# Kernel optimization log

Hardware: AMD Instinct MI355X
Metric: run time of the kernel (lower is better)

Reference implementation:

```python
import jax, jax.numpy as jnp
import numpy as np

H = 8        # heads
W = 64       # window size
SHIFT = True
DIM = 512
SCALE = (DIM // H) ** -0.5


def setup_inputs() -> dict:
    key = jax.random.key(0)
    k1, k2, k3, k4 = jax.random.split(key, 4)
    x = jax.random.normal(k1, (8, 4096, DIM), dtype=jnp.float32)
    w_qkv = jax.random.normal(k2, (3 * DIM, DIM), dtype=jnp.float32) * 0.02
    w_proj = jax.random.normal(k3, (DIM, DIM), dtype=jnp.float32) * 0.02
    b_proj = jax.random.normal(k4, (DIM,), dtype=jnp.float32) * 0.02
    return {"x": x, "w_qkv": w_qkv, "w_proj": w_proj, "b_proj": b_proj}


def reference(x, w_qkv, w_proj, b_proj):
    B, N, C = x.shape
    if SHIFT:
        x = jnp.roll(x, -W // 2, axis=1)
    pad = (W - N % W) % W  # static Python int
    if pad:
        x = jnp.pad(x, ((0, 0), (0, pad), (0, 0)))
    nw = x.shape[1] // W
    xw = x.reshape(B * nw, W, C)                     # (B', W, C)
    qkv = xw @ w_qkv.T                               # (B', W, 3C)
    qkv = qkv.reshape(B * nw, W, 3, H, C // H)
    q, k, v = qkv[:, :, 0], qkv[:, :, 1], qkv[:, :, 2]  # (B', W, H, dh)
    # NOTE: faithful to source -- heads are NOT moved before matmul, so
    # attention is over the head axis: attn shape (B', W, H, H).
    attn = jnp.einsum('bwhd,bwgd->bwhg', q, k) * SCALE
    attn = jax.nn.softmax(attn, axis=-1)
    out = jnp.einsum('bwhg,bwgd->bwhd', attn, v)     # (B', W, H, dh)
    # transpose(1,2) then raw reshape, exactly as torch does (channel scramble)
    out = out.transpose(0, 2, 1, 3).reshape(B * nw, W, C)
    out = out @ w_proj.T + b_proj
    out = out.reshape(B, nw * W, C)[:, :N]
    if SHIFT:
        out = jnp.roll(out, W // 2, axis=1)
    return out
```

## Files before the change

kernel.cpp:

```cpp
#include <hip/hip_runtime.h>
#include <math.h>

typedef __attribute__((ext_vector_type(8))) short short8;
typedef __attribute__((ext_vector_type(4))) float float4v;

#define KDIM  512
#define NQKV  1536

__device__ __forceinline__ unsigned short f2bf(float f) {
    unsigned int u = __float_as_uint(f);
    u += 0x7FFFu + ((u >> 16) & 1u);
    return (unsigned short)(u >> 16);
}
__device__ __forceinline__ float bf2f(unsigned short u) {
    return __uint_as_float(((unsigned int)u) << 16);
}

__device__ __forceinline__ void gl2lds16(const unsigned short* g, unsigned short* l) {
    __builtin_amdgcn_global_load_lds(
        (const __attribute__((address_space(1))) void*)g,
        (__attribute__((address_space(3))) void*)l, 16, 0, 0);
}

__global__ __launch_bounds__(256) void cast_all_kernel(const float* __restrict__ x,
                                                       const float* __restrict__ wqkv,
                                                       const float* __restrict__ wproj,
                                                       unsigned short* __restrict__ xb,
                                                       unsigned short* __restrict__ wqkvb,
                                                       unsigned short* __restrict__ wprojb) {
    if (blockIdx.x < 16384) {
        int tid = blockIdx.x * 256 + threadIdx.x;
        int t = tid >> 7;
        int c = (tid & 127) << 2;
        int b = t >> 12, n = t & 4095;
        int src = (b << 12) | ((n + 32) & 4095);
        float4 v = *(const float4*)(x + (((size_t)src) << 9) + c);
        ushort4 o;
        o.x = f2bf(v.x); o.y = f2bf(v.y); o.z = f2bf(v.z); o.w = f2bf(v.w);
        *(ushort4*)(xb + (((size_t)t) << 9) + c) = o;
    } else {
        int tid = (blockIdx.x - 16384) * 256 + threadIdx.x;
        int e = tid << 2;
        if (e < NQKV * KDIM) {
            float4 v = *(const float4*)(wqkv + e);
            ushort4 o; o.x = f2bf(v.x); o.y = f2bf(v.y); o.z = f2bf(v.z); o.w = f2bf(v.w);
            *(ushort4*)(wqkvb + e) = o;
        } else {
            int e2 = e - NQKV * KDIM;
            float4 v = *(const float4*)(wproj + e2);
            ushort4 o; o.x = f2bf(v.x); o.y = f2bf(v.y); o.z = f2bf(v.z); o.w = f2bf(v.w);
            *(ushort4*)(wprojb + e2) = o;
        }
    }
}

template<int N>
__global__ __launch_bounds__(256, 2) void gemm_kernel(
        const unsigned short* __restrict__ A,
        const unsigned short* __restrict__ B,
        unsigned short* __restrict__ Cb) {
    __shared__ __align__(16) unsigned short As[128 * 64];
    __shared__ __align__(16) unsigned short Bs[128 * 64];
    constexpr int GX  = N / 128;
    constexpr int PER = (GX * 256) / 8;
    const int wgid = blockIdx.y * GX + blockIdx.x;
    const int swz  = (wgid & 7) * PER + (wgid >> 3);
    const int bm = swz / GX;
    const int bn = swz % GX;

    const int tid = threadIdx.x;
    const int wave = tid >> 6, lane = tid & 63;
    const int quad = lane >> 4, l16 = lane & 15;
    const int wm = (wave >> 1) * 64, wn = (wave & 1) * 64;
    const int srow = lane >> 3;
    const int scol = ((lane & 7) ^ srow) * 8;

    float4v acc[4][4] = {};

    const unsigned short* Abase = A + (size_t)(bm * 128) * KDIM;
    const unsigned short* Bbase = B + (size_t)(bn * 128) * KDIM;

    for (int k0 = 0; k0 < KDIM; k0 += 64) {
        #pragma unroll
        for (int j = 0; j < 4; j++) {
            int chunk = j * 4 + wave;
            int row = chunk * 8 + srow;
            gl2lds16(Abase + (size_t)row * KDIM + k0 + scol, As + chunk * 512);
            gl2lds16(Bbase + (size_t)row * KDIM + k0 + scol, Bs + chunk * 512);
        }
        __syncthreads();
        #pragma unroll
        for (int ki = 0; ki < 2; ki++) {
            short8 af[4], bf[4];
            #pragma unroll
            for (int mi = 0; mi < 4; mi++) {
                int r = wm + mi * 16 + l16;
                int blk = (ki * 4 + quad) ^ (l16 & 7);
                af[mi] = *(const short8*)(As + r * 64 + blk * 8);
            }
            #pragma unroll
            for (int ni = 0; ni < 4; ni++) {
                int r = wn + ni * 16 + l16;
                int blk = (ki * 4 + quad) ^ (l16 & 7);
                bf[ni] = *(const short8*)(Bs + r * 64 + blk * 8);
            }
            #pragma unroll
            for (int mi = 0; mi < 4; mi++)
                #pragma unroll
                for (int ni = 0; ni < 4; ni++)
                    acc[mi][ni] = __builtin_amdgcn_mfma_f32_16x16x32_bf16(
                        af[mi], bf[ni], acc[mi][ni], 0, 0, 0);
        }
        __syncthreads();
    }

    #pragma unroll
    for (int mi = 0; mi < 4; mi++) {
        #pragma unroll
        for (int r = 0; r < 4; r++) {
            int m = bm * 128 + wm + mi * 16 + quad * 4 + r;
            #pragma unroll
            for (int ni = 0; ni < 4; ni++) {
                int n = bn * 128 + wn + ni * 16 + l16;
                Cb[(size_t)m * N + n] = f2bf(acc[mi][ni][r]);
            }
        }
    }
}

#define KVS 1032
__global__ __launch_bounds__(512, 4) void attnproj_kernel(
        const unsigned short* __restrict__ qkvb,
        const unsigned short* __restrict__ wprojb,
        const float* __restrict__ bias,
        float* __restrict__ out) {
    __shared__ __align__(16) unsigned short Asf[32 * 512];
    __shared__ __align__(16) unsigned short KV[16 * KVS];
    const int tid = threadIdx.x;
    const int bid = blockIdx.x;
    const int swzb = (bid & 7) * 128 + (bid >> 3);
    const int win = swzb >> 1, half = swzb & 1;

    {
        const int dq = tid & 7;
        const int h  = (tid >> 3) & 3;
        const int tl = tid >> 5;
        const int hg = half * 4 + h;

        short8 qs[4];
        #pragma unroll
        for (int c = 0; c < 4; c++)
            qs[c] = *(const short8*)(qkvb + (size_t)(win * 64 + c * 16 + tl) * NQKV
                                     + hg * 64 + dq * 8);

        #pragma unroll
        for (int c = 0; c < 4; c++) {
            #pragma unroll
            for (int i = 0; i < 4; i++) {
                int slot = i * 512 + tid;
                int row = slot >> 7, c8 = slot & 127;
                gl2lds16(qkvb + (size_t)(win * 64 + c * 16 + row) * NQKV + 512 + c8 * 8,
                         KV + row * KVS + c8 * 8);
            }
            __syncthreads();

            const unsigned short* krow = KV + tl * KVS;
            const int w = c * 16 + tl;

            float qv[8];
            #pragma unroll
            for (int j = 0; j < 8; j++)
                qv[j] = bf2f((unsigned short)qs[c][j]);

            float s[8];
            #pragma unroll
            for (int g = 0; g < 8; g++) {
                float acc = 0.f;
                short8 ks = *(const short8*)(krow + g * 64 + dq * 8);
                #pragma unroll
                for (int j = 0; j < 8; j++)
                    acc += qv[j] * bf2f((unsigned short)ks[j]);
                acc += __shfl_xor(acc, 1);
                acc += __shfl_xor(acc, 2);
                acc += __shfl_xor(acc, 4);
                s[g] = acc;
            }

            float mx = s[0];
            #pragma unroll
            for (int g = 1; g < 8; g++) mx = fmaxf(mx, s[g]);
            float p[8], sum = 0.f;
            #pragma unroll
            for (int g = 0; g < 8; g++) { p[g] = __expf((s[g] - mx) * 0.125f); sum += p[g]; }
            float inv = 1.f / sum;
            #pragma unroll
            for (int g = 0; g < 8; g++) p[g] *= inv;

            float o[8];
            #pragma unroll
            for (int j = 0; j < 8; j++) o[j] = 0.f;
            #pragma unroll
            for (int g = 0; g < 8; g++) {
                short8 vs = *(const short8*)(krow + 512 + g * 64 + dq * 8);
                #pragma unroll
                for (int j = 0; j < 8; j++)
                    o[j] += p[g] * bf2f((unsigned short)vs[j]);
            }

            int r = h * 8 + (w >> 3);
            int keyr = (r ^ (r >> 3)) & 7;
            short8 pk;
            #pragma unroll
            for (int j = 0; j < 8; j++) pk[j] = (short)f2bf(o[j]);
            int cb = (w & 7) * 8 + dq;
            *(short8*)(Asf + r * 512 + ((cb ^ keyr) * 8)) = pk;
            __syncthreads();
        }
    }

    const int wave = tid >> 6, lane = tid & 63;
    const int quad = lane >> 4, l16 = lane & 15;
    const int wc = wave;

    float4v acc[2][4] = {};
    #pragma unroll
    for (int ks = 0; ks < 16; ks++) {
        short8 af[2], bfr[4];
        #pragma unroll
        for (int mi = 0; mi < 2; mi++) {
            int r = mi * 16 + l16;
            int kb = ks * 4 + quad;
            af[mi] = *(const short8*)(Asf + r * 512 + ((kb ^ ((r ^ (r >> 3)) & 7)) * 8));
        }
        #pragma unroll
        for (int ni = 0; ni < 4; ni++) {
            int r = wc * 64 + ni * 16 + l16;
            bfr[ni] = *(const short8*)(wprojb + (size_t)r * KDIM + ks * 32 + quad * 8);
        }
        #pragma unroll
        for (int mi = 0; mi < 2; mi++)
            #pragma unroll
            for (int ni = 0; ni < 4; ni++)
                acc[mi][ni] = __builtin_amdgcn_mfma_f32_16x16x32_bf16(
                    af[mi], bfr[ni], acc[mi][ni], 0, 0, 0);
    }

    #pragma unroll
    for (int mi = 0; mi < 2; mi++) {
        #pragma unroll
        for (int r4 = 0; r4 < 4; r4++) {
            int m = win * 64 + half * 32 + mi * 16 + quad * 4 + r4;
            int b = m >> 12, pp = m & 4095;
            int nrow = (pp + 32) & 4095;
            float* orow = out + (((size_t)((b << 12) | nrow)) << 9);
            #pragma unroll
            for (int ni = 0; ni < 4; ni++) {
                int n = wc * 64 + ni * 16 + l16;
                orow[n] = acc[mi][ni][r4] + bias[n];
            }
        }
    }
}

extern "C" void kernel_launch(void* const* d_in, const int* in_sizes, int n_in,
                              void* d_out, int out_size, void* d_ws, size_t ws_size,
                              hipStream_t stream) {
    const float* x      = (const float*)d_in[0];
    const float* w_qkv  = (const float*)d_in[1];
    const float* w_proj = (const float*)d_in[2];
    const float* b_proj = (const float*)d_in[3];
    float* out = (float*)d_out;

    char* ws = (char*)d_ws;
    unsigned short* xb     = (unsigned short*)(ws);
    unsigned short* wqkvb  = (unsigned short*)(ws + 33554432);
    unsigned short* wprojb = (unsigned short*)(ws + 35127296);
    unsigned short* qkvb   = (unsigned short*)(ws + 35651584);

    cast_all_kernel<<<17408, 256, 0, stream>>>(x, w_qkv, w_proj, xb, wqkvb, wprojb);
    gemm_kernel<NQKV><<<dim3(12, 256), 256, 0, stream>>>(xb, wqkvb, qkvb);
    attnproj_kernel<<<1024, 512, 0, stream>>>(qkvb, wprojb, b_proj, out);
}
```

Baseline: 256.5 us.

## Process whole window per block, interleaving attention and projection per chunk

Each block now handles one whole 64-token window with all 8 heads instead of half a window, so K/V rows are loaded once rather than twice. Attention output for each 16-token chunk is projected right away through a 16-row MFMA GEMM, and the next chunk's K/V load to LDS is issued before that GEMM so the two overlap. K/V LDS rows are XOR-swizzled instead of padded, and bias is hoisted into registers. The cost is half as many blocks, more register use, and reloading w_proj from global once per chunk.

```diff
diff --git a/kernel.cpp b/kernel.cpp
--- a/kernel.cpp
+++ b/kernel.cpp
@@ -128,137 +128,149 @@
     }
 }
 
-#define KVS 1032
 __global__ __launch_bounds__(512, 4) void attnproj_kernel(
         const unsigned short* __restrict__ qkvb,
         const unsigned short* __restrict__ wprojb,
         const float* __restrict__ bias,
         float* __restrict__ out) {
-    __shared__ __align__(16) unsigned short Asf[32 * 512];
-    __shared__ __align__(16) unsigned short KV[16 * KVS];
+    __shared__ __align__(16) unsigned short Asf[16 * 512];
+    __shared__ __align__(16) unsigned short KV[16 * 1024];
     const int tid = threadIdx.x;
     const int bid = blockIdx.x;
-    const int swzb = (bid & 7) * 128 + (bid >> 3);
-    const int win = swzb >> 1, half = swzb & 1;
-
-    {
-        const int dq = tid & 7;
-        const int h  = (tid >> 3) & 3;
-        const int tl = tid >> 5;
-        const int hg = half * 4 + h;
-
-        short8 qs[4];
-        #pragma unroll
-        for (int c = 0; c < 4; c++)
-            qs[c] = *(const short8*)(qkvb + (size_t)(win * 64 + c * 16 + tl) * NQKV
-                                     + hg * 64 + dq * 8);
-
-        #pragma unroll
-        for (int c = 0; c < 4; c++) {
-            #pragma unroll
-            for (int i = 0; i < 4; i++) {
-                int slot = i * 512 + tid;
-                int row = slot >> 7, c8 = slot & 127;
-                gl2lds16(qkvb + (size_t)(win * 64 + c * 16 + row) * NQKV + 512 + c8 * 8,
-                         KV + row * KVS + c8 * 8);
-            }
-            __syncthreads();
-
-            const unsigned short* krow = KV + tl * KVS;
-            const int w = c * 16 + tl;
-
-            float qv[8];
-            #pragma unroll
-            for (int j = 0; j < 8; j++)
-                qv[j] = bf2f((unsigned short)qs[c][j]);
-
-            float s[8];
-            #pragma unroll
-            for (int g = 0; g < 8; g++) {
-                float acc = 0.f;
-                short8 ks = *(const short8*)(krow + g * 64 + dq * 8);
-                #pragma unroll
-                for (int j = 0; j < 8; j++)
-                    acc += qv[j] * bf2f((unsigned short)ks[j]);
-                acc += __shfl_xor(acc, 1);
-                acc += __shfl_xor(acc, 2);
-                acc += __shfl_xor(acc, 4);
-                s[g] = acc;
-            }
-
-            float mx = s[0];
-            #pragma unroll
-            for (int g = 1; g < 8; g++) mx = fmaxf(mx, s[g]);
-            float p[8], sum = 0.f;
-            #pragma unroll
-            for (int g = 0; g < 8; g++) { p[g] = __expf((s[g] - mx) * 0.125f); sum += p[g]; }
-            float inv = 1.f / sum;
-            #pragma unroll
-            for (int g = 0; g < 8; g++) p[g] *= inv;
-
-            float o[8];
-            #pragma unroll
-            for (int j = 0; j < 8; j++) o[j] = 0.f;
-            #pragma unroll
-            for (int g = 0; g < 8; g++) {
-                short8 vs = *(const short8*)(krow + 512 + g * 64 + dq * 8);
-                #pragma unroll
-                for (int j = 0; j < 8; j++)
-                    o[j] += p[g] * bf2f((unsigned short)vs[j]);
-            }
-
-            int r = h * 8 + (w >> 3);
-            int keyr = (r ^ (r >> 3)) & 7;
-            short8 pk;
-            #pragma unroll
-            for (int j = 0; j < 8; j++) pk[j] = (short)f2bf(o[j]);
-            int cb = (w & 7) * 8 + dq;
-            *(short8*)(Asf + r * 512 + ((cb ^ keyr) * 8)) = pk;
-            __syncthreads();
-        }
-    }
+    const int win = (bid & 7) * 64 + (bid >> 3);
+
+    const int dq = tid & 3;
+    const int h  = (tid >> 2) & 7;
+    const int tl = tid >> 5;
+    const int tkey = tl & 7;
 
     const int wave = tid >> 6, lane = tid & 63;
     const int quad = lane >> 4, l16 = lane & 15;
-    const int wc = wave;
-
-    float4v acc[2][4] = {};
-    #pragma unroll
-    for (int ks = 0; ks < 16; ks++) {
-        short8 af[2], bfr[4];
-        #pragma unroll
-        for (int mi = 0; mi < 2; mi++) {
-            int r = mi * 16 + l16;
+
+    short8 q0[4], q1[4];
+    #pragma unroll
+    for (int c = 0; c < 4; c++) {
+        const unsigned short* qsrc =
+            qkvb + (size_t)(win * 64 + c * 16 + tl) * NQKV + h * 64 + dq * 16;
+        q0[c] = *(const short8*)qsrc;
+        q1[c] = *(const short8*)(qsrc + 8);
+    }
+    float bias_r[4];
+    #pragma unroll
+    for (int ni = 0; ni < 4; ni++)
+        bias_r[ni] = bias[wave * 64 + ni * 16 + l16];
+
+    #pragma unroll
+    for (int i = 0; i < 4; i++) {
+        int slot = i * 512 + tid, row = slot >> 7, u = slot & 127;
+        gl2lds16(qkvb + (size_t)(win * 64 + row) * NQKV + 512 + (u ^ (row & 7)) * 8,
+                 KV + row * 1024 + u * 8);
+    }
+    __syncthreads();
+
+    #pragma unroll
+    for (int c = 0; c < 4; c++) {
+        float qv[16];
+        #pragma unroll
+        for (int j = 0; j < 8; j++) {
+            qv[j]     = bf2f((unsigned short)q0[c][j]);
+            qv[8 + j] = bf2f((unsigned short)q1[c][j]);
+        }
+        const unsigned short* krow = KV + tl * 1024;
+
+        float s[8];
+        #pragma unroll
+        for (int g = 0; g < 8; g++) {
+            int lu = g * 8 + dq * 2;
+            short8 k0 = *(const short8*)(krow + ((lu ^ tkey) * 8));
+            short8 k1 = *(const short8*)(krow + (((lu + 1) ^ tkey) * 8));
+            float acc = 0.f;
+            #pragma unroll
+            for (int j = 0; j < 8; j++)
+                acc += qv[j] * bf2f((unsigned short)k0[j])
+                     + qv[8 + j] * bf2f((unsigned short)k1[j]);
+            acc += __shfl_xor(acc, 1);
+            acc += __shfl_xor(acc, 2);
+            s[g] = acc;
+        }
+
+        float mx = s[0];
+        #pragma unroll
+        for (int g = 1; g < 8; g++) mx = fmaxf(mx, s[g]);
+        float p[8], sum = 0.f;
+        #pragma unroll
+        for (int g = 0; g < 8; g++) { p[g] = __expf((s[g] - mx) * 0.125f); sum += p[g]; }
+        float inv = 1.f / sum;
+        #pragma unroll
+        for (int g = 0; g < 8; g++) p[g] *= inv;
+
+        float o[16];
+        #pragma unroll
+        for (int j = 0; j < 16; j++) o[j] = 0.f;
+        #pragma unroll
+        for (int g = 0; g < 8; g++) {
+            int lu = 64 + g * 8 + dq * 2;
+            short8 v0 = *(const short8*)(krow + ((lu ^ tkey) * 8));
+            short8 v1 = *(const short8*)(krow + (((lu + 1) ^ tkey) * 8));
+            #pragma unroll
+            for (int j = 0; j < 8; j++) {
+                o[j]     += p[g] * bf2f((unsigned short)v0[j]);
+                o[8 + j] += p[g] * bf2f((unsigned short)v1[j]);
+            }
+        }
+
+        {
+            int lr = h * 2 + (tl >> 3);
+            int key2 = (lr ^ (lr >> 3)) & 7;
+            int cb = tkey * 8 + dq * 2;
+            short8 pk0, pk1;
+            #pragma unroll
+            for (int j = 0; j < 8; j++) {
+                pk0[j] = (short)f2bf(o[j]);
+                pk1[j] = (short)f2bf(o[8 + j]);
+            }
+            *(short8*)(Asf + lr * 512 + ((cb ^ key2) * 8)) = pk0;
+            *(short8*)(Asf + lr * 512 + (((cb + 1) ^ key2) * 8)) = pk1;
+        }
+        __syncthreads();
+
+        if (c < 3) {
+            #pragma unroll
+            for (int i = 0; i < 4; i++) {
+                int slot = i * 512 + tid, row = slot >> 7, u = slot & 127;
+                gl2lds16(qkvb + (size_t)(win * 64 + (c + 1) * 16 + row) * NQKV
+                                + 512 + (u ^ (row & 7)) * 8,
+                         KV + row * 1024 + u * 8);
+            }
+        }
+
+        float4v acc2[4] = {};
+        #pragma unroll
+        for (int ks = 0; ks < 16; ks++) {
             int kb = ks * 4 + quad;
-            af[mi] = *(const short8*)(Asf + r * 512 + ((kb ^ ((r ^ (r >> 3)) & 7)) * 8));
-        }
-        #pragma unroll
-        for (int ni = 0; ni < 4; ni++) {
-            int r = wc * 64 + ni * 16 + l16;
-            bfr[ni] = *(const short8*)(wprojb + (size_t)r * KDIM + ks * 32 + quad * 8);
-        }
-        #pragma unroll
-        for (int mi = 0; mi < 2; mi++)
-            #pragma unroll
-            for (int ni = 0; ni < 4; ni++)
-                acc[mi][ni] = __builtin_amdgcn_mfma_f32_16x16x32_bf16(
-                    af[mi], bfr[ni], acc[mi][ni], 0, 0, 0);
-    }
-
-    #pragma unroll
-    for (int mi = 0; mi < 2; mi++) {
+            short8 af = *(const short8*)(Asf + l16 * 512 +
+                            ((kb ^ ((l16 ^ (l16 >> 3)) & 7)) * 8));
+            #pragma unroll
+            for (int ni = 0; ni < 4; ni++) {
+                short8 bfr = *(const short8*)(wprojb +
+                    (size_t)(wave * 64 + ni * 16 + l16) * KDIM + ks * 32 + quad * 8);
+                acc2[ni] = __builtin_amdgcn_mfma_f32_16x16x32_bf16(
+                    af, bfr, acc2[ni], 0, 0, 0);
+            }
+        }
+
         #pragma unroll
         for (int r4 = 0; r4 < 4; r4++) {
-            int m = win * 64 + half * 32 + mi * 16 + quad * 4 + r4;
-            int b = m >> 12, pp = m & 4095;
+            int lr2 = quad * 4 + r4;
+            int gm = win * 64 + (lr2 >> 1) * 8 + 2 * c + (lr2 & 1);
+            int b = gm >> 12, pp = gm & 4095;
             int nrow = (pp + 32) & 4095;
             float* orow = out + (((size_t)((b << 12) | nrow)) << 9);
             #pragma unroll
-            for (int ni = 0; ni < 4; ni++) {
-                int n = wc * 64 + ni * 16 + l16;
-                orow[n] = acc[mi][ni][r4] + bias[n];
-            }
-        }
+            for (int ni = 0; ni < 4; ni++)
+                orow[wave * 64 + ni * 16 + l16] = acc2[ni][r4] + bias_r[ni];
+        }
+        __syncthreads();
     }
 }
 
@@ -279,5 +291,5 @@
 
     cast_all_kernel<<<17408, 256, 0, stream>>>(x, w_qkv, w_proj, xb, wqkvb, wprojb);
     gemm_kernel<NQKV><<<dim3(12, 256), 256, 0, stream>>>(xb, wqkvb, qkvb);
-    attnproj_kernel<<<1024, 512, 0, stream>>>(qkvb, wprojb, b_proj, out);
-}
+    attnproj_kernel<<<512, 512, 0, stream>>>(qkvb, wprojb, b_proj, out);
+}
```

After: 432.0 us. +68.4%, slower.
